# Performance work log

Measured on AMD Instinct MI355X. Metric: run time of the kernel, lower is better.

## Reference

```python
import jax, jax.numpy as jnp
import numpy as np

E, B, DX, DC, DH, DO = 16, 4096, 128, 64, 1024, 128
DIN = DX + DC

def setup_inputs() -> dict:
    key = jax.random.key(0)
    ks = jax.random.split(key, 6)
    s1 = 1.0 / np.sqrt(DIN)
    s2 = 1.0 / np.sqrt(DH)
    return {
        "x": jax.random.normal(ks[0], (E, B, DX), dtype=jnp.float32),
        "cond": jax.random.normal(ks[1], (E, B, DC), dtype=jnp.float32),
        # stacked per-expert params, mirroring param_stacks ([E, ...])
        "W1": jax.random.uniform(ks[2], (E, DH, DIN), minval=-s1, maxval=s1, dtype=jnp.float32),
        "b1": jax.random.uniform(ks[3], (E, DH), minval=-s1, maxval=s1, dtype=jnp.float32),
        "W2": jax.random.uniform(ks[4], (E, DO, DH), minval=-s2, maxval=s2, dtype=jnp.float32),
        "b2": jax.random.uniform(ks[5], (E, DO), minval=-s2, maxval=s2, dtype=jnp.float32),
    }

def reference(x, cond, W1, b1, W2, b2):
    # vmap over experts == grouped GEMM with per-expert weight tiles
    xc = jnp.concatenate([x, cond], axis=-1)          # [E, B, DIN]
    h = jnp.einsum('ebi,ehi->ebh', xc, W1) + b1[:, None, :]  # [E, B, DH]
    h = jax.nn.relu(h)
    y = jnp.einsum('ebh,eoh->ebo', h, W2) + b2[:, None, :]   # [E, B, DO]
    return y
```

## Files before the change

### kernel.cpp

```cpp
#include <hip/hip_runtime.h>
#include <hip/hip_bf16.h>

#define E_   16
#define B_   4096
#define DX_  128
#define DC_  64
#define DIN_ 192
#define DH_  1024
#define DO_  128

#define BM 256
#define KC 64
#define NCHUNK (DH_ / KC)
#define NT 512

#define W1B_OFF 0
#define W1B_STR 12288
#define W2B_OFF 24576
#define W2B_STR 8192
#define HB_OFF  40960
#define HB_STR  16384

typedef __attribute__((ext_vector_type(4))) float f32x4;
typedef __attribute__((ext_vector_type(8))) short bf16x8;

__device__ __forceinline__ unsigned f2bf_u(float f) {
    union { float f; unsigned u; } v; v.f = f;
    return (v.u + 0x7fffu + ((v.u >> 16) & 1u)) >> 16;
}
__device__ __forceinline__ uint2 pack4(float4 v) {
    uint2 r;
    r.x = f2bf_u(v.x) | (f2bf_u(v.y) << 16);
    r.y = f2bf_u(v.z) | (f2bf_u(v.w) << 16);
    return r;
}
__device__ __forceinline__ int swz(int r, int S, int cb) {
    return r * S + ((cb ^ ((r & 7) << 4)) >> 1);
}

__global__ __launch_bounds__(NT, 2)
void moe_fused_kernel(const float* __restrict__ x, const float* __restrict__ cond,
                      const float* __restrict__ W1, const float* __restrict__ b1,
                      const float* __restrict__ W2, const float* __restrict__ b2,
                      float* __restrict__ out) {
    __shared__ short LDSU[73728];

    const int bid = blockIdx.x;
    const int xcd = bid & 7;
    const int s   = bid >> 3;
    const int e   = 2 * xcd + (s & 1);
    const int row0 = (s >> 1) * BM;

    const int tid  = threadIdx.x;
    const int w    = tid >> 6;
    const int lane = tid & 63;
    const int lr   = lane & 15;
    const int lg   = lane >> 4;
    const int band = w * 32;
    const int wr   = w >> 1, wc2 = w & 1;

    const float4* g1base = (const float4*)(W1 + (size_t)e * DH_ * DIN_);

    float4 r1[6];
#pragma unroll
    for (int i = 0; i < 6; ++i) r1[i] = g1base[tid + NT * i];

    {
        const float4* gx = (const float4*)(x + (size_t)(e * B_ + row0) * DX_);
#pragma unroll
        for (int i = 0; i < 16; ++i) {
            int g = tid + NT * i;
            int r = g >> 5, c = g & 31;
            *(uint2*)&LDSU[swz(r, DIN_, c * 8)] = pack4(gx[g]);
        }
        const float4* gc = (const float4*)(cond + (size_t)(e * B_ + row0) * DC_);
#pragma unroll
        for (int i = 0; i < 8; ++i) {
            int g = tid + NT * i;
            int r = g >> 4, c = g & 15;
            *(uint2*)&LDSU[128 + swz(r, DIN_, c * 8)] = pack4(gc[g]);
        }
    }
    __syncthreads();

    bf16x8 xcreg[2][6];
#pragma unroll
    for (int mf = 0; mf < 2; ++mf)
#pragma unroll
        for (int kk = 0; kk < 6; ++kk)
            xcreg[mf][kk] = *(const bf16x8*)&LDSU[swz(band + mf * 16 + lr, DIN_, kk * 64 + lg * 16)];
    __syncthreads();

#pragma unroll
    for (int i = 0; i < 6; ++i) {
        int g = tid + NT * i;
        int r = g / 48, cc = g - r * 48;
        *(uint2*)&LDSU[W1B_OFF + swz(r, DIN_, cc * 8)] = pack4(r1[i]);
    }
#pragma unroll
    for (int i = 0; i < 6; ++i)
        r1[i] = g1base[(KC * DIN_ / 4) + tid + NT * i];
    float4 r2[4];
    {
        const float* g2 = W2 + (size_t)e * DO_ * DH_;
#pragma unroll
        for (int i = 0; i < 4; ++i) {
            int g = tid + NT * i;
            int r = g >> 4, cc = g & 15;
            r2[i] = *(const float4*)(g2 + (size_t)r * DH_ + cc * 4);
        }
    }
    __syncthreads();

    f32x4 acc2[4][4] = {};

    for (int c = 0; c < NCHUNK; ++c) {
        const int pc = c & 1, pp = pc ^ 1;

        float b1v[4];
#pragma unroll
        for (int nf = 0; nf < 4; ++nf)
            b1v[nf] = b1[e * DH_ + c * KC + nf * 16 + lr];

#pragma unroll
        for (int i = 0; i < 4; ++i) {
            int g = tid + NT * i;
            int r = g >> 4, cc = g & 15;
            *(uint2*)&LDSU[W2B_OFF + pc * W2B_STR + swz(r, KC, cc * 8)] = pack4(r2[i]);
        }
        if (c + 1 < NCHUNK) {
#pragma unroll
            for (int i = 0; i < 6; ++i) {
                int g = tid + NT * i;
                int r = g / 48, cc = g - r * 48;
                *(uint2*)&LDSU[W1B_OFF + pp * W1B_STR + swz(r, DIN_, cc * 8)] = pack4(r1[i]);
            }
        }
        if (c + 2 < NCHUNK) {
#pragma unroll
            for (int i = 0; i < 6; ++i)
                r1[i] = g1base[(c + 2) * (KC * DIN_ / 4) + tid + NT * i];
        }
        if (c + 1 < NCHUNK) {
            const float* g2 = W2 + (size_t)e * DO_ * DH_ + (size_t)(c + 1) * KC;
#pragma unroll
            for (int i = 0; i < 4; ++i) {
                int g = tid + NT * i;
                int r = g >> 4, cc = g & 15;
                r2[i] = *(const float4*)(g2 + (size_t)r * DH_ + cc * 4);
            }
        }

        if (c > 0) {
#pragma unroll
            for (int kk = 0; kk < KC / 32; ++kk) {
                bf16x8 af[4], bfr[4];
#pragma unroll
                for (int mf = 0; mf < 4; ++mf) {
                    int r = wr * 64 + mf * 16 + lr;
                    af[mf] = *(const bf16x8*)&LDSU[HB_OFF + pp * HB_STR + swz(r, KC, kk * 64 + lg * 16)];
                }
#pragma unroll
                for (int nf = 0; nf < 4; ++nf) {
                    int r = wc2 * 64 + nf * 16 + lr;
                    bfr[nf] = *(const bf16x8*)&LDSU[W2B_OFF + pp * W2B_STR + swz(r, KC, kk * 64 + lg * 16)];
                }
#pragma unroll
                for (int mf = 0; mf < 4; ++mf)
#pragma unroll
                    for (int nf = 0; nf < 4; ++nf)
                        acc2[mf][nf] = __builtin_amdgcn_mfma_f32_16x16x32_bf16(af[mf], bfr[nf], acc2[mf][nf], 0, 0, 0);
            }
        }

        f32x4 acc1[2][4] = {};
#pragma unroll
        for (int kk = 0; kk < DIN_ / 32; ++kk) {
            bf16x8 bfr[4];
#pragma unroll
            for (int nf = 0; nf < 4; ++nf) {
                int r = nf * 16 + lr;
                bfr[nf] = *(const bf16x8*)&LDSU[W1B_OFF + pc * W1B_STR + swz(r, DIN_, kk * 64 + lg * 16)];
            }
#pragma unroll
            for (int mf = 0; mf < 2; ++mf)
#pragma unroll
                for (int nf = 0; nf < 4; ++nf)
                    acc1[mf][nf] = __builtin_amdgcn_mfma_f32_16x16x32_bf16(xcreg[mf][kk], bfr[nf], acc1[mf][nf], 0, 0, 0);
        }
#pragma unroll
        for (int mf = 0; mf < 2; ++mf)
#pragma unroll
            for (int nf = 0; nf < 4; ++nf)
#pragma unroll
                for (int j = 0; j < 4; ++j) {
                    float v = fmaxf(acc1[mf][nf][j] + b1v[nf], 0.f);
                    int hr = band + mf * 16 + lg * 4 + j;
                    int hc = nf * 16 + lr;
                    LDSU[HB_OFF + pc * HB_STR + swz(hr, KC, 2 * hc)] = (short)f2bf_u(v);
                }

        __syncthreads();
    }

    {
        const int pl = (NCHUNK - 1) & 1;
#pragma unroll
        for (int kk = 0; kk < KC / 32; ++kk) {
            bf16x8 af[4], bfr[4];
#pragma unroll
            for (int mf = 0; mf < 4; ++mf) {
                int r = wr * 64 + mf * 16 + lr;
                af[mf] = *(const bf16x8*)&LDSU[HB_OFF + pl * HB_STR + swz(r, KC, kk * 64 + lg * 16)];
            }
#pragma unroll
            for (int nf = 0; nf < 4; ++nf) {
                int r = wc2 * 64 + nf * 16 + lr;
                bfr[nf] = *(const bf16x8*)&LDSU[W2B_OFF + pl * W2B_STR + swz(r, KC, kk * 64 + lg * 16)];
            }
#pragma unroll
            for (int mf = 0; mf < 4; ++mf)
#pragma unroll
                for (int nf = 0; nf < 4; ++nf)
                    acc2[mf][nf] = __builtin_amdgcn_mfma_f32_16x16x32_bf16(af[mf], bfr[nf], acc2[mf][nf], 0, 0, 0);
        }
    }

    float b2v[4];
#pragma unroll
    for (int nf = 0; nf < 4; ++nf)
        b2v[nf] = b2[e * DO_ + wc2 * 64 + nf * 16 + lr];
#pragma unroll
    for (int mf = 0; mf < 4; ++mf)
#pragma unroll
        for (int nf = 0; nf < 4; ++nf)
#pragma unroll
            for (int j = 0; j < 4; ++j) {
                int m = wr * 64 + mf * 16 + lg * 4 + j;
                int o = wc2 * 64 + nf * 16 + lr;
                out[(size_t)(e * B_ + row0 + m) * DO_ + o] = acc2[mf][nf][j] + b2v[nf];
            }
}

extern "C" void kernel_launch(void* const* d_in, const int* in_sizes, int n_in,
                              void* d_out, int out_size, void* d_ws, size_t ws_size,
                              hipStream_t stream) {
    const float* x    = (const float*)d_in[0];
    const float* cond = (const float*)d_in[1];
    const float* W1   = (const float*)d_in[2];
    const float* b1   = (const float*)d_in[3];
    const float* W2   = (const float*)d_in[4];
    const float* b2   = (const float*)d_in[5];
    float* out = (float*)d_out;

    dim3 grid(E_ * (B_ / BM));
    dim3 block(NT);
    moe_fused_kernel<<<grid, block, 0, stream>>>(x, cond, W1, b1, W2, b2, out);
}
```

Baseline: 193.0 us.

## Pre-convert weights to bf16 in workspace and double block size to 1024 threads

```diff
diff --git a/kernel.cpp b/kernel.cpp
--- a/kernel.cpp
+++ b/kernel.cpp
@@ -12,7 +12,7 @@
 #define BM 256
 #define KC 64
 #define NCHUNK (DH_ / KC)
-#define NT 512
+#define NT 1024
 
 #define W1B_OFF 0
 #define W1B_STR 12288
@@ -21,6 +21,10 @@
 #define HB_OFF  40960
 #define HB_STR  16384
 
+#define NW1U2 (E_ * DH_ * DIN_ / 4)
+#define NW2U2 (E_ * DO_ * DH_ / 4)
+#define WS_BYTES ((size_t)(NW1U2 + NW2U2) * 8)
+
 typedef __attribute__((ext_vector_type(4))) float f32x4;
 typedef __attribute__((ext_vector_type(8))) short bf16x8;
 
@@ -38,11 +42,22 @@
     return r * S + ((cb ^ ((r & 7) << 4)) >> 1);
 }
 
-__global__ __launch_bounds__(NT, 2)
+__global__ __launch_bounds__(256)
+void convert_w(const float4* __restrict__ W1, const float4* __restrict__ W2,
+               uint2* __restrict__ ws) {
+    const int ntot = NW1U2 + NW2U2;
+    for (int i = blockIdx.x * 256 + threadIdx.x; i < ntot; i += gridDim.x * 256) {
+        float4 v = (i < NW1U2) ? W1[i] : W2[i - NW1U2];
+        ws[i] = pack4(v);
+    }
+}
+
+template <bool WS>
+__global__ __launch_bounds__(NT, 4)
 void moe_fused_kernel(const float* __restrict__ x, const float* __restrict__ cond,
                       const float* __restrict__ W1, const float* __restrict__ b1,
                       const float* __restrict__ W2, const float* __restrict__ b2,
-                      float* __restrict__ out) {
+                      const uint2* __restrict__ wsw, float* __restrict__ out) {
     __shared__ short LDSU[73728];
 
     const int bid = blockIdx.x;
@@ -56,26 +71,35 @@
     const int lane = tid & 63;
     const int lr   = lane & 15;
     const int lg   = lane >> 4;
-    const int band = w * 32;
-    const int wr   = w >> 1, wc2 = w & 1;
-
-    const float4* g1base = (const float4*)(W1 + (size_t)e * DH_ * DIN_);
-
-    float4 r1[6];
-#pragma unroll
-    for (int i = 0; i < 6; ++i) r1[i] = g1base[tid + NT * i];
+    const int wr   = w >> 2, wc2 = w & 3;
+
+    const uint2*  ws1 = wsw + (size_t)e * (DH_ * DIN_ / 4);
+    const uint2*  ws2 = wsw + NW1U2 + (size_t)e * (DO_ * DH_ / 4);
+    const float4* g1f = (const float4*)(W1 + (size_t)e * DH_ * DIN_);
+    const float*  g2f = W2 + (size_t)e * DO_ * DH_;
+
+    uint2 r1[3]; float4 r1f[3];
+    uint2 r2[2]; float4 r2f[2];
+
+    if constexpr (WS) {
+#pragma unroll
+        for (int i = 0; i < 3; ++i) r1[i] = ws1[tid + NT * i];
+    } else {
+#pragma unroll
+        for (int i = 0; i < 3; ++i) r1f[i] = g1f[tid + NT * i];
+    }
 
     {
         const float4* gx = (const float4*)(x + (size_t)(e * B_ + row0) * DX_);
 #pragma unroll
-        for (int i = 0; i < 16; ++i) {
+        for (int i = 0; i < 8; ++i) {
             int g = tid + NT * i;
             int r = g >> 5, c = g & 31;
             *(uint2*)&LDSU[swz(r, DIN_, c * 8)] = pack4(gx[g]);
         }
         const float4* gc = (const float4*)(cond + (size_t)(e * B_ + row0) * DC_);
 #pragma unroll
-        for (int i = 0; i < 8; ++i) {
+        for (int i = 0; i < 4; ++i) {
             int g = tid + NT * i;
             int r = g >> 4, c = g & 15;
             *(uint2*)&LDSU[128 + swz(r, DIN_, c * 8)] = pack4(gc[g]);
@@ -83,36 +107,41 @@
     }
     __syncthreads();
 
-    bf16x8 xcreg[2][6];
-#pragma unroll
-    for (int mf = 0; mf < 2; ++mf)
-#pragma unroll
-        for (int kk = 0; kk < 6; ++kk)
-            xcreg[mf][kk] = *(const bf16x8*)&LDSU[swz(band + mf * 16 + lr, DIN_, kk * 64 + lg * 16)];
+    bf16x8 xcreg[6];
+#pragma unroll
+    for (int kk = 0; kk < 6; ++kk)
+        xcreg[kk] = *(const bf16x8*)&LDSU[swz(w * 16 + lr, DIN_, kk * 64 + lg * 16)];
     __syncthreads();
 
 #pragma unroll
-    for (int i = 0; i < 6; ++i) {
+    for (int i = 0; i < 3; ++i) {
         int g = tid + NT * i;
         int r = g / 48, cc = g - r * 48;
-        *(uint2*)&LDSU[W1B_OFF + swz(r, DIN_, cc * 8)] = pack4(r1[i]);
-    }
-#pragma unroll
-    for (int i = 0; i < 6; ++i)
-        r1[i] = g1base[(KC * DIN_ / 4) + tid + NT * i];
-    float4 r2[4];
-    {
-        const float* g2 = W2 + (size_t)e * DO_ * DH_;
-#pragma unroll
-        for (int i = 0; i < 4; ++i) {
+        uint2 pv; if constexpr (WS) pv = r1[i]; else pv = pack4(r1f[i]);
+        *(uint2*)&LDSU[W1B_OFF + swz(r, DIN_, cc * 8)] = pv;
+    }
+    if constexpr (WS) {
+#pragma unroll
+        for (int i = 0; i < 3; ++i) r1[i] = ws1[3072 + tid + NT * i];
+#pragma unroll
+        for (int i = 0; i < 2; ++i) {
             int g = tid + NT * i;
             int r = g >> 4, cc = g & 15;
-            r2[i] = *(const float4*)(g2 + (size_t)r * DH_ + cc * 4);
+            r2[i] = ws2[r * 256 + cc];
+        }
+    } else {
+#pragma unroll
+        for (int i = 0; i < 3; ++i) r1f[i] = g1f[3072 + tid + NT * i];
+#pragma unroll
+        for (int i = 0; i < 2; ++i) {
+            int g = tid + NT * i;
+            int r = g >> 4, cc = g & 15;
+            r2f[i] = *(const float4*)(g2f + (size_t)r * DH_ + cc * 4);
         }
     }
     __syncthreads();
 
-    f32x4 acc2[4][4] = {};
+    f32x4 acc2[4][2] = {};
 
     for (int c = 0; c < NCHUNK; ++c) {
         const int pc = c & 1, pp = pc ^ 1;
@@ -123,82 +152,86 @@
             b1v[nf] = b1[e * DH_ + c * KC + nf * 16 + lr];
 
 #pragma unroll
-        for (int i = 0; i < 4; ++i) {
+        for (int i = 0; i < 2; ++i) {
             int g = tid + NT * i;
             int r = g >> 4, cc = g & 15;
-            *(uint2*)&LDSU[W2B_OFF + pc * W2B_STR + swz(r, KC, cc * 8)] = pack4(r2[i]);
+            uint2 pv; if constexpr (WS) pv = r2[i]; else pv = pack4(r2f[i]);
+            *(uint2*)&LDSU[W2B_OFF + pc * W2B_STR + swz(r, KC, cc * 8)] = pv;
         }
         if (c + 1 < NCHUNK) {
 #pragma unroll
-            for (int i = 0; i < 6; ++i) {
+            for (int i = 0; i < 3; ++i) {
                 int g = tid + NT * i;
                 int r = g / 48, cc = g - r * 48;
-                *(uint2*)&LDSU[W1B_OFF + pp * W1B_STR + swz(r, DIN_, cc * 8)] = pack4(r1[i]);
+                uint2 pv; if constexpr (WS) pv = r1[i]; else pv = pack4(r1f[i]);
+                *(uint2*)&LDSU[W1B_OFF + pp * W1B_STR + swz(r, DIN_, cc * 8)] = pv;
             }
         }
         if (c + 2 < NCHUNK) {
-#pragma unroll
-            for (int i = 0; i < 6; ++i)
-                r1[i] = g1base[(c + 2) * (KC * DIN_ / 4) + tid + NT * i];
+            if constexpr (WS) {
+#pragma unroll
+                for (int i = 0; i < 3; ++i) r1[i] = ws1[(c + 2) * 3072 + tid + NT * i];
+            } else {
+#pragma unroll
+                for (int i = 0; i < 3; ++i) r1f[i] = g1f[(c + 2) * 3072 + tid + NT * i];
+            }
         }
         if (c + 1 < NCHUNK) {
-            const float* g2 = W2 + (size_t)e * DO_ * DH_ + (size_t)(c + 1) * KC;
-#pragma unroll
-            for (int i = 0; i < 4; ++i) {
-                int g = tid + NT * i;
-                int r = g >> 4, cc = g & 15;
-                r2[i] = *(const float4*)(g2 + (size_t)r * DH_ + cc * 4);
+            if constexpr (WS) {
+#pragma unroll
+                for (int i = 0; i < 2; ++i) {
+                    int g = tid + NT * i;
+                    int r = g >> 4, cc = g & 15;
+                    r2[i] = ws2[r * 256 + (c + 1) * 16 + cc];
+                }
+            } else {
+#pragma unroll
+                for (int i = 0; i < 2; ++i) {
+                    int g = tid + NT * i;
+                    int r = g >> 4, cc = g & 15;
+                    r2f[i] = *(const float4*)(g2f + (size_t)r * DH_ + (c + 1) * KC + cc * 4);
+                }
             }
         }
 
         if (c > 0) {
 #pragma unroll
             for (int kk = 0; kk < KC / 32; ++kk) {
-                bf16x8 af[4], bfr[4];
-#pragma unroll
-                for (int mf = 0; mf < 4; ++mf) {
-                    int r = wr * 64 + mf * 16 + lr;
-                    af[mf] = *(const bf16x8*)&LDSU[HB_OFF + pp * HB_STR + swz(r, KC, kk * 64 + lg * 16)];
-                }
-#pragma unroll
-                for (int nf = 0; nf < 4; ++nf) {
-                    int r = wc2 * 64 + nf * 16 + lr;
-                    bfr[nf] = *(const bf16x8*)&LDSU[W2B_OFF + pp * W2B_STR + swz(r, KC, kk * 64 + lg * 16)];
-                }
+                bf16x8 af[4], bfr[2];
 #pragma unroll
                 for (int mf = 0; mf < 4; ++mf)
-#pragma unroll
-                    for (int nf = 0; nf < 4; ++nf)
+                    af[mf] = *(const bf16x8*)&LDSU[HB_OFF + pp * HB_STR + swz(wr * 64 + mf * 16 + lr, KC, kk * 64 + lg * 16)];
+#pragma unroll
+                for (int nf = 0; nf < 2; ++nf)
+                    bfr[nf] = *(const bf16x8*)&LDSU[W2B_OFF + pp * W2B_STR + swz(wc2 * 32 + nf * 16 + lr, KC, kk * 64 + lg * 16)];
+#pragma unroll
+                for (int mf = 0; mf < 4; ++mf)
+#pragma unroll
+                    for (int nf = 0; nf < 2; ++nf)
                         acc2[mf][nf] = __builtin_amdgcn_mfma_f32_16x16x32_bf16(af[mf], bfr[nf], acc2[mf][nf], 0, 0, 0);
             }
         }
 
-        f32x4 acc1[2][4] = {};
+        f32x4 acc1[4] = {};
 #pragma unroll
         for (int kk = 0; kk < DIN_ / 32; ++kk) {
             bf16x8 bfr[4];
 #pragma unroll
-            for (int nf = 0; nf < 4; ++nf) {
-                int r = nf * 16 + lr;
-                bfr[nf] = *(const bf16x8*)&LDSU[W1B_OFF + pc * W1B_STR + swz(r, DIN_, kk * 64 + lg * 16)];
-            }
-#pragma unroll
-            for (int mf = 0; mf < 2; ++mf)
-#pragma unroll
-                for (int nf = 0; nf < 4; ++nf)
-                    acc1[mf][nf] = __builtin_amdgcn_mfma_f32_16x16x32_bf16(xcreg[mf][kk], bfr[nf], acc1[mf][nf], 0, 0, 0);
-        }
-#pragma unroll
-        for (int mf = 0; mf < 2; ++mf)
-#pragma unroll
             for (int nf = 0; nf < 4; ++nf)
-#pragma unroll
-                for (int j = 0; j < 4; ++j) {
-                    float v = fmaxf(acc1[mf][nf][j] + b1v[nf], 0.f);
-                    int hr = band + mf * 16 + lg * 4 + j;
-                    int hc = nf * 16 + lr;
-                    LDSU[HB_OFF + pc * HB_STR + swz(hr, KC, 2 * hc)] = (short)f2bf_u(v);
-                }
+                bfr[nf] = *(const bf16x8*)&LDSU[W1B_OFF + pc * W1B_STR + swz(nf * 16 + lr, DIN_, kk * 64 + lg * 16)];
+#pragma unroll
+            for (int nf = 0; nf < 4; ++nf)
+                acc1[nf] = __builtin_amdgcn_mfma_f32_16x16x32_bf16(xcreg[kk], bfr[nf], acc1[nf], 0, 0, 0);
+        }
+#pragma unroll
+        for (int nf = 0; nf < 4; ++nf)
+#pragma unroll
+            for (int j = 0; j < 4; ++j) {
+                float v = fmaxf(acc1[nf][j] + b1v[nf], 0.f);
+                int hr = w * 16 + lg * 4 + j;
+                int hc = nf * 16 + lr;
+                LDSU[HB_OFF + pc * HB_STR + swz(hr, KC, 2 * hc)] = (short)f2bf_u(v);
+            }
 
         __syncthreads();
     }
@@ -207,37 +240,33 @@
         const int pl = (NCHUNK - 1) & 1;
 #pragma unroll
         for (int kk = 0; kk < KC / 32; ++kk) {
-            bf16x8 af[4], bfr[4];
-#pragma unroll
-            for (int mf = 0; mf < 4; ++mf) {
-                int r = wr * 64 + mf * 16 + lr;
-                af[mf] = *(const bf16x8*)&LDSU[HB_OFF + pl * HB_STR + swz(r, KC, kk * 64 + lg * 16)];
-            }
-#pragma unroll
-            for (int nf = 0; nf < 4; ++nf) {
-                int r = wc2 * 64 + nf * 16 + lr;
-                bfr[nf] = *(const bf16x8*)&LDSU[W2B_OFF + pl * W2B_STR + swz(r, KC, kk * 64 + lg * 16)];
-            }
+            bf16x8 af[4], bfr[2];
 #pragma unroll
             for (int mf = 0; mf < 4; ++mf)
-#pragma unroll
-                for (int nf = 0; nf < 4; ++nf)
+                af[mf] = *(const bf16x8*)&LDSU[HB_OFF + pl * HB_STR + swz(wr * 64 + mf * 16 + lr, KC, kk * 64 + lg * 16)];
+#pragma unroll
+            for (int nf = 0; nf < 2; ++nf)
+                bfr[nf] = *(const bf16x8*)&LDSU[W2B_OFF + pl * W2B_STR + swz(wc2 * 32 + nf * 16 + lr, KC, kk * 64 + lg * 16)];
+#pragma unroll
+            for (int mf = 0; mf < 4; ++mf)
+#pragma unroll
+                for (int nf = 0; nf < 2; ++nf)
                     acc2[mf][nf] = __builtin_amdgcn_mfma_f32_16x16x32_bf16(af[mf], bfr[nf], acc2[mf][nf], 0, 0, 0);
         }
     }
 
-    float b2v[4];
-#pragma unroll
-    for (int nf = 0; nf < 4; ++nf)
-        b2v[nf] = b2[e * DO_ + wc2 * 64 + nf * 16 + lr];
+    float b2v[2];
+#pragma unroll
+    for (int nf = 0; nf < 2; ++nf)
+        b2v[nf] = b2[e * DO_ + wc2 * 32 + nf * 16 + lr];
 #pragma unroll
     for (int mf = 0; mf < 4; ++mf)
 #pragma unroll
-        for (int nf = 0; nf < 4; ++nf)
+        for (int nf = 0; nf < 2; ++nf)
 #pragma unroll
             for (int j = 0; j < 4; ++j) {
                 int m = wr * 64 + mf * 16 + lg * 4 + j;
-                int o = wc2 * 64 + nf * 16 + lr;
+                int o = wc2 * 32 + nf * 16 + lr;
                 out[(size_t)(e * B_ + row0 + m) * DO_ + o] = acc2[mf][nf][j] + b2v[nf];
             }
 }
@@ -255,5 +284,15 @@
 
     dim3 grid(E_ * (B_ / BM));
     dim3 block(NT);
-    moe_fused_kernel<<<grid, block, 0, stream>>>(x, cond, W1, b1, W2, b2, out);
-}
+
+    const bool usews = (ws_size >= WS_BYTES) && (d_ws != nullptr);
+    if (usews) {
+        convert_w<<<2560, 256, 0, stream>>>((const float4*)W1, (const float4*)W2,
+                                            (uint2*)d_ws);
+        moe_fused_kernel<true><<<grid, block, 0, stream>>>(
+            x, cond, W1, b1, W2, b2, (const uint2*)d_ws, out);
+    } else {
+        moe_fused_kernel<false><<<grid, block, 0, stream>>>(
+            x, cond, W1, b1, W2, b2, (const uint2*)nullptr, out);
+    }
+}
```

New measurement: 170.9 us. -11.4%, faster.
